# Kernel optimization log

Measured on AMD Instinct MI355X. Metric: run time of the kernel, lower is better.

The kernel has to match this reference:

```python
import jax, jax.numpy as jnp
import numpy as np


def setup_inputs() -> dict:
    key = jax.random.key(0)
    k1, k2, k3 = jax.random.split(key, 3)
    B, S, Q, K, D = 64, 512, 800, 4, 64
    q_data = jax.random.normal(k1, (B, S, Q), dtype=jnp.float32)
    r_data = jax.random.randint(k2, (B, S), 0, K)
    # learned params (xavier-ish scale)
    Wq = jax.random.normal(k3, (D, Q), dtype=jnp.float32) * (0.5 * (2.0 / (Q + D)) ** 0.5)
    bq = jnp.zeros((D,), dtype=jnp.float32)
    Wr = jax.random.normal(jax.random.fold_in(key, 7), (1, K), dtype=jnp.float32) * (0.5 * (2.0 / (K + 1)) ** 0.5)
    br = jnp.zeros((1,), dtype=jnp.float32)
    return {"q_data": q_data, "r_data": r_data, "Wq": Wq, "bq": bq,
            "Wr": Wr, "br": br, "n_questions": Q, "n_cats": K}


def reference(q_data, r_data, Wq, bq, Wr, br, n_questions, n_cats):
    # Vectorized over (batch, seq): original looped over t in python.
    K = n_cats
    k_idx = jnp.arange(K, dtype=q_data.dtype)                      # [K]
    dist = jnp.abs(k_idx[None, None, :] - r_data[..., None].astype(q_data.dtype)) / (K - 1)  # [B,S,K]
    weights = jnp.maximum(1.0 - dist, 0.0)                        # [B,S,K]
    # response_weights: Linear(K -> 1) then sigmoid -> scalar gate per (b,s)
    gate = jax.nn.sigmoid(jnp.einsum('bsk,ok->bso', weights, Wr) + br)  # [B,S,1]
    weighted_q = q_data * gate                                    # [B,S,Q]
    # question_embed: Linear(Q -> D)
    out = jnp.einsum('bsq,dq->bsd', weighted_q, Wq) + bq          # [B,S,D]
    return out
```

## Files before the change

### kernel.cpp

```cpp
#include <hip/hip_runtime.h>
#include <hip/hip_bf16.h>


#define QD 800
#define DD 64
#define M_TOTAL 32768
#define KT 25
#define DEPTH 5

typedef __attribute__((ext_vector_type(8))) short bf16x8;
typedef __attribute__((ext_vector_type(4))) float f32x4;

static __device__ __forceinline__ short f2bf(float f) {
  union { __hip_bfloat16 h; short s; } u;
  u.h = __float2bfloat16(f);
  return u.s;
}

static __device__ __forceinline__ bf16x8 pack8(f32x4 lo, f32x4 hi) {
  bf16x8 r;
  r[0] = f2bf(lo.x); r[1] = f2bf(lo.y); r[2] = f2bf(lo.z); r[3] = f2bf(lo.w);
  r[4] = f2bf(hi.x); r[5] = f2bf(hi.y); r[6] = f2bf(hi.z); r[7] = f2bf(hi.w);
  return r;
}

static __device__ __forceinline__ bf16x8 load_split8(const float* __restrict__ p) {
  return pack8(*reinterpret_cast<const f32x4*>(p),
               *reinterpret_cast<const f32x4*>(p + 16));
}

__global__ void convert_wq_kernel(const float* __restrict__ Wq, short* __restrict__ Bb) {
  int idx = blockIdx.x * 256 + threadIdx.x;
  int kt = idx >> 8;
  int acc = (idx >> 6) & 3;
  int lane = idx & 63;
  int l15 = lane & 15, lhi = lane >> 4;
  const float* p = Wq + (acc * 16 + l15) * QD + kt * 32 + lhi * 4;
  *reinterpret_cast<bf16x8*>(Bb + (size_t)idx * 8) = load_split8(p);
}

__global__ __launch_bounds__(256, 2) void sold_kernel(
    const float* __restrict__ q, const int* __restrict__ rdat,
    const short* __restrict__ Bb, const float* __restrict__ bq,
    const float* __restrict__ Wr, const float* __restrict__ br,
    float* __restrict__ out) {
  const int lane = threadIdx.x & 63;
  const int wave = threadIdx.x >> 6;
  const int l15 = lane & 15;
  const int lhi = lane >> 4;
  const int m0 = blockIdx.x * 64 + wave * 16;

  const float* ap = q + (size_t)(m0 + l15) * QD + lhi * 4;
  const short* bp = Bb + (size_t)lane * 8;

  f32x4 aLo[DEPTH], aHi[DEPTH];
  bf16x8 bfr[DEPTH][4];

#pragma unroll
  for (int s = 0; s < DEPTH; ++s) {
    const float* a = ap + s * 32;
    aLo[s] = *reinterpret_cast<const f32x4*>(a);
    aHi[s] = *reinterpret_cast<const f32x4*>(a + 16);
    const short* p = bp + s * 2048;
    bfr[s][0] = *reinterpret_cast<const bf16x8*>(p + 0 * 512);
    bfr[s][1] = *reinterpret_cast<const bf16x8*>(p + 1 * 512);
    bfr[s][2] = *reinterpret_cast<const bf16x8*>(p + 2 * 512);
    bfr[s][3] = *reinterpret_cast<const bf16x8*>(p + 3 * 512);
  }

  f32x4 acc0 = {0.f, 0.f, 0.f, 0.f};
  f32x4 acc1 = {0.f, 0.f, 0.f, 0.f};
  f32x4 acc2 = {0.f, 0.f, 0.f, 0.f};
  f32x4 acc3 = {0.f, 0.f, 0.f, 0.f};

#pragma unroll
  for (int kt = 0; kt < KT; ++kt) {
    const int s = kt % DEPTH;
    bf16x8 a = pack8(aLo[s], aHi[s]);
    acc0 = __builtin_amdgcn_mfma_f32_16x16x32_bf16(a, bfr[s][0], acc0, 0, 0, 0);
    acc1 = __builtin_amdgcn_mfma_f32_16x16x32_bf16(a, bfr[s][1], acc1, 0, 0, 0);
    acc2 = __builtin_amdgcn_mfma_f32_16x16x32_bf16(a, bfr[s][2], acc2, 0, 0, 0);
    acc3 = __builtin_amdgcn_mfma_f32_16x16x32_bf16(a, bfr[s][3], acc3, 0, 0, 0);
    const int nx = kt + DEPTH;
    if (nx < KT) {
      const float* a2 = ap + nx * 32;
      aLo[s] = *reinterpret_cast<const f32x4*>(a2);
      aHi[s] = *reinterpret_cast<const f32x4*>(a2 + 16);
      const short* p = bp + nx * 2048;
      bfr[s][0] = *reinterpret_cast<const bf16x8*>(p + 0 * 512);
      bfr[s][1] = *reinterpret_cast<const bf16x8*>(p + 1 * 512);
      bfr[s][2] = *reinterpret_cast<const bf16x8*>(p + 2 * 512);
      bfr[s][3] = *reinterpret_cast<const bf16x8*>(p + 3 * 512);
    }
    __builtin_amdgcn_sched_barrier(0);
  }

  float wr[4] = {Wr[0], Wr[1], Wr[2], Wr[3]};
  float brv = br[0];
  float lut[4];
  const float inv3 = 1.0f / 3.0f;
#pragma unroll
  for (int r = 0; r < 4; ++r) {
    float s = brv;
#pragma unroll
    for (int k = 0; k < 4; ++k) {
      float w = fmaxf(1.0f - fabsf((float)(k - r)) * inv3, 0.0f);
      s += w * wr[k];
    }
    lut[r] = 1.0f / (1.0f + __expf(-s));
  }

  float bqv0 = bq[0 * 16 + l15];
  float bqv1 = bq[1 * 16 + l15];
  float bqv2 = bq[2 * 16 + l15];
  float bqv3 = bq[3 * 16 + l15];

#pragma unroll
  for (int r = 0; r < 4; ++r) {
    int row = m0 + lhi * 4 + r;
    float g = lut[rdat[row]];
    float* orow = out + (size_t)row * DD + l15;
    orow[0]  = acc0[r] * g + bqv0;
    orow[16] = acc1[r] * g + bqv1;
    orow[32] = acc2[r] * g + bqv2;
    orow[48] = acc3[r] * g + bqv3;
  }
}

__global__ __launch_bounds__(256, 2) void sold_direct(
    const float* __restrict__ q, const int* __restrict__ rdat,
    const float* __restrict__ Wq, const float* __restrict__ bq,
    const float* __restrict__ Wr, const float* __restrict__ br,
    float* __restrict__ out) {
  const int lane = threadIdx.x & 63;
  const int wave = threadIdx.x >> 6;
  const int l15 = lane & 15;
  const int lhi = lane >> 4;
  const int m0 = blockIdx.x * 64 + wave * 16;
  const float* aptr = q + (size_t)(m0 + l15) * QD + lhi * 4;
  const float* w0 = Wq + (0 * 16 + l15) * QD + lhi * 4;
  const float* w1 = Wq + (1 * 16 + l15) * QD + lhi * 4;
  const float* w2 = Wq + (2 * 16 + l15) * QD + lhi * 4;
  const float* w3 = Wq + (3 * 16 + l15) * QD + lhi * 4;
  f32x4 acc0 = {0.f,0.f,0.f,0.f}, acc1 = {0.f,0.f,0.f,0.f};
  f32x4 acc2 = {0.f,0.f,0.f,0.f}, acc3 = {0.f,0.f,0.f,0.f};
#pragma unroll 5
  for (int kt = 0; kt < KT; ++kt) {
    bf16x8 a  = load_split8(aptr + kt * 32);
    bf16x8 b0 = load_split8(w0 + kt * 32);
    bf16x8 b1 = load_split8(w1 + kt * 32);
    bf16x8 b2 = load_split8(w2 + kt * 32);
    bf16x8 b3 = load_split8(w3 + kt * 32);
    acc0 = __builtin_amdgcn_mfma_f32_16x16x32_bf16(a, b0, acc0, 0, 0, 0);
    acc1 = __builtin_amdgcn_mfma_f32_16x16x32_bf16(a, b1, acc1, 0, 0, 0);
    acc2 = __builtin_amdgcn_mfma_f32_16x16x32_bf16(a, b2, acc2, 0, 0, 0);
    acc3 = __builtin_amdgcn_mfma_f32_16x16x32_bf16(a, b3, acc3, 0, 0, 0);
  }
  float wr[4] = {Wr[0], Wr[1], Wr[2], Wr[3]};
  float brv = br[0], lut[4];
  const float inv3 = 1.0f / 3.0f;
#pragma unroll
  for (int r = 0; r < 4; ++r) {
    float s = brv;
#pragma unroll
    for (int k = 0; k < 4; ++k)
      s += fmaxf(1.0f - fabsf((float)(k - r)) * inv3, 0.0f) * wr[k];
    lut[r] = 1.0f / (1.0f + __expf(-s));
  }
  float bqv0 = bq[l15], bqv1 = bq[16 + l15], bqv2 = bq[32 + l15], bqv3 = bq[48 + l15];
#pragma unroll
  for (int r = 0; r < 4; ++r) {
    int row = m0 + lhi * 4 + r;
    float g = lut[rdat[row]];
    float* orow = out + (size_t)row * DD + l15;
    orow[0]  = acc0[r] * g + bqv0;
    orow[16] = acc1[r] * g + bqv1;
    orow[32] = acc2[r] * g + bqv2;
    orow[48] = acc3[r] * g + bqv3;
  }
}

extern "C" void kernel_launch(void* const* d_in, const int* in_sizes, int n_in,
                              void* d_out, int out_size, void* d_ws, size_t ws_size,
                              hipStream_t stream) {
  const float* q    = (const float*)d_in[0];
  const int*   rdat = (const int*)d_in[1];
  const float* Wq   = (const float*)d_in[2];
  const float* bq   = (const float*)d_in[3];
  const float* Wr   = (const float*)d_in[4];
  const float* br   = (const float*)d_in[5];
  float* out = (float*)d_out;

  const size_t need_ws = (size_t)KT * 2048 * sizeof(short);
  if (ws_size >= need_ws) {
    short* Bb = (short*)d_ws;
    convert_wq_kernel<<<KT, 256, 0, stream>>>(Wq, Bb);
    sold_kernel<<<M_TOTAL / 64, 256, 0, stream>>>(q, rdat, Bb, bq, Wr, br, out);
  } else {
    sold_direct<<<M_TOTAL / 64, 256, 0, stream>>>(q, rdat, Wq, bq, Wr, br, out);
  }
}
```

Before: 169.8 us.

## Split K across two waves per block with 4x4 MFMA tiles and LDS reduction

Each block now uses two waves instead of four. Each wave computes all 64 rows by 64 columns of the block's output tile over half of the K dimension, using 16 accumulators so every loaded B fragment is reused across four row tiles. The two partial sums are combined through shared memory before the gated epilogue. The aim is to cut redundant B-fragment loads, but the change raises register pressure, lowers the wave count per CU, and adds a sync plus a reduction through shared memory.

```diff
diff --git a/kernel.cpp b/kernel.cpp
--- a/kernel.cpp
+++ b/kernel.cpp
@@ -6,7 +6,8 @@
 #define DD 64
 #define M_TOTAL 32768
 #define KT 25
-#define DEPTH 5
+#define KSPLIT 13
+#define DEPTH 3
 
 typedef __attribute__((ext_vector_type(8))) short bf16x8;
 typedef __attribute__((ext_vector_type(4))) float f32x4;
@@ -32,68 +33,111 @@
 __global__ void convert_wq_kernel(const float* __restrict__ Wq, short* __restrict__ Bb) {
   int idx = blockIdx.x * 256 + threadIdx.x;
   int kt = idx >> 8;
-  int acc = (idx >> 6) & 3;
+  int c = (idx >> 6) & 3;
   int lane = idx & 63;
   int l15 = lane & 15, lhi = lane >> 4;
-  const float* p = Wq + (acc * 16 + l15) * QD + kt * 32 + lhi * 4;
+  const float* p = Wq + (c * 16 + l15) * QD + kt * 32 + lhi * 4;
   *reinterpret_cast<bf16x8*>(Bb + (size_t)idx * 8) = load_split8(p);
 }
 
-__global__ __launch_bounds__(256, 2) void sold_kernel(
+template <int CNT>
+static __device__ __forceinline__ void pipe_loop(
+    const float* __restrict__ a0, const float* __restrict__ a1,
+    const float* __restrict__ a2, const float* __restrict__ a3,
+    const short* __restrict__ bp, f32x4 (&acc)[4][4]) {
+  const float* at[4] = {a0, a1, a2, a3};
+  f32x4 sAlo[DEPTH][4], sAhi[DEPTH][4];
+  bf16x8 sB[DEPTH][4];
+
+#pragma unroll
+  for (int s = 0; s < DEPTH; ++s) {
+    if (s < CNT) {
+#pragma unroll
+      for (int t = 0; t < 4; ++t) {
+        sAlo[s][t] = *reinterpret_cast<const f32x4*>(at[t] + s * 32);
+        sAhi[s][t] = *reinterpret_cast<const f32x4*>(at[t] + s * 32 + 16);
+      }
+#pragma unroll
+      for (int c = 0; c < 4; ++c)
+        sB[s][c] = *reinterpret_cast<const bf16x8*>(bp + s * 2048 + c * 512);
+    }
+  }
+
+#pragma unroll
+  for (int kt = 0; kt < CNT; ++kt) {
+    const int s = kt % DEPTH;
+    bf16x8 afr[4];
+#pragma unroll
+    for (int t = 0; t < 4; ++t) afr[t] = pack8(sAlo[s][t], sAhi[s][t]);
+#pragma unroll
+    for (int t = 0; t < 4; ++t)
+#pragma unroll
+      for (int c = 0; c < 4; ++c)
+        acc[t][c] = __builtin_amdgcn_mfma_f32_16x16x32_bf16(afr[t], sB[s][c],
+                                                            acc[t][c], 0, 0, 0);
+    const int nx = kt + DEPTH;
+    if (nx < CNT) {
+#pragma unroll
+      for (int t = 0; t < 4; ++t) {
+        sAlo[s][t] = *reinterpret_cast<const f32x4*>(at[t] + nx * 32);
+        sAhi[s][t] = *reinterpret_cast<const f32x4*>(at[t] + nx * 32 + 16);
+      }
+#pragma unroll
+      for (int c = 0; c < 4; ++c)
+        sB[s][c] = *reinterpret_cast<const bf16x8*>(bp + nx * 2048 + c * 512);
+    }
+    __builtin_amdgcn_sched_barrier(0);
+  }
+}
+
+__global__ __launch_bounds__(128, 1) void sold_kernel(
     const float* __restrict__ q, const int* __restrict__ rdat,
     const short* __restrict__ Bb, const float* __restrict__ bq,
     const float* __restrict__ Wr, const float* __restrict__ br,
     float* __restrict__ out) {
   const int lane = threadIdx.x & 63;
-  const int wave = threadIdx.x >> 6;
+  const int khalf = threadIdx.x >> 6;
   const int l15 = lane & 15;
   const int lhi = lane >> 4;
-  const int m0 = blockIdx.x * 64 + wave * 16;
-
-  const float* ap = q + (size_t)(m0 + l15) * QD + lhi * 4;
-  const short* bp = Bb + (size_t)lane * 8;
-
-  f32x4 aLo[DEPTH], aHi[DEPTH];
-  bf16x8 bfr[DEPTH][4];
-
-#pragma unroll
-  for (int s = 0; s < DEPTH; ++s) {
-    const float* a = ap + s * 32;
-    aLo[s] = *reinterpret_cast<const f32x4*>(a);
-    aHi[s] = *reinterpret_cast<const f32x4*>(a + 16);
-    const short* p = bp + s * 2048;
-    bfr[s][0] = *reinterpret_cast<const bf16x8*>(p + 0 * 512);
-    bfr[s][1] = *reinterpret_cast<const bf16x8*>(p + 1 * 512);
-    bfr[s][2] = *reinterpret_cast<const bf16x8*>(p + 2 * 512);
-    bfr[s][3] = *reinterpret_cast<const bf16x8*>(p + 3 * 512);
-  }
-
-  f32x4 acc0 = {0.f, 0.f, 0.f, 0.f};
-  f32x4 acc1 = {0.f, 0.f, 0.f, 0.f};
-  f32x4 acc2 = {0.f, 0.f, 0.f, 0.f};
-  f32x4 acc3 = {0.f, 0.f, 0.f, 0.f};
-
-#pragma unroll
-  for (int kt = 0; kt < KT; ++kt) {
-    const int s = kt % DEPTH;
-    bf16x8 a = pack8(aLo[s], aHi[s]);
-    acc0 = __builtin_amdgcn_mfma_f32_16x16x32_bf16(a, bfr[s][0], acc0, 0, 0, 0);
-    acc1 = __builtin_amdgcn_mfma_f32_16x16x32_bf16(a, bfr[s][1], acc1, 0, 0, 0);
-    acc2 = __builtin_amdgcn_mfma_f32_16x16x32_bf16(a, bfr[s][2], acc2, 0, 0, 0);
-    acc3 = __builtin_amdgcn_mfma_f32_16x16x32_bf16(a, bfr[s][3], acc3, 0, 0, 0);
-    const int nx = kt + DEPTH;
-    if (nx < KT) {
-      const float* a2 = ap + nx * 32;
-      aLo[s] = *reinterpret_cast<const f32x4*>(a2);
-      aHi[s] = *reinterpret_cast<const f32x4*>(a2 + 16);
-      const short* p = bp + nx * 2048;
-      bfr[s][0] = *reinterpret_cast<const bf16x8*>(p + 0 * 512);
-      bfr[s][1] = *reinterpret_cast<const bf16x8*>(p + 1 * 512);
-      bfr[s][2] = *reinterpret_cast<const bf16x8*>(p + 2 * 512);
-      bfr[s][3] = *reinterpret_cast<const bf16x8*>(p + 3 * 512);
-    }
-    __builtin_amdgcn_sched_barrier(0);
-  }
+  const int m0 = blockIdx.x * 64;
+  const int kt0 = khalf ? KSPLIT : 0;
+
+  const float* a0 = q + (size_t)(m0 +  0 + l15) * QD + kt0 * 32 + lhi * 4;
+  const float* a1 = q + (size_t)(m0 + 16 + l15) * QD + kt0 * 32 + lhi * 4;
+  const float* a2 = q + (size_t)(m0 + 32 + l15) * QD + kt0 * 32 + lhi * 4;
+  const float* a3 = q + (size_t)(m0 + 48 + l15) * QD + kt0 * 32 + lhi * 4;
+  const short* bp = Bb + (size_t)kt0 * 2048 + lane * 8;
+
+  f32x4 acc[4][4];
+#pragma unroll
+  for (int t = 0; t < 4; ++t)
+#pragma unroll
+    for (int c = 0; c < 4; ++c) acc[t][c] = {0.f, 0.f, 0.f, 0.f};
+
+  if (khalf == 0) {
+    pipe_loop<KSPLIT>(a0, a1, a2, a3, bp, acc);
+  } else {
+    pipe_loop<KT - KSPLIT>(a0, a1, a2, a3, bp, acc);
+  }
+
+  __shared__ float comb[4][16][64];
+  if (khalf == 1) {
+#pragma unroll
+    for (int t = 0; t < 4; ++t)
+#pragma unroll
+      for (int c = 0; c < 4; ++c)
+#pragma unroll
+        for (int r = 0; r < 4; ++r) comb[t][c * 4 + r][lane] = acc[t][c][r];
+  }
+  __syncthreads();
+  if (khalf == 1) return;
+
+#pragma unroll
+  for (int t = 0; t < 4; ++t)
+#pragma unroll
+    for (int c = 0; c < 4; ++c)
+#pragma unroll
+      for (int r = 0; r < 4; ++r) acc[t][c][r] += comb[t][c * 4 + r][lane];
 
   float wr[4] = {Wr[0], Wr[1], Wr[2], Wr[3]};
   float brv = br[0];
@@ -103,27 +147,25 @@
   for (int r = 0; r < 4; ++r) {
     float s = brv;
 #pragma unroll
-    for (int k = 0; k < 4; ++k) {
-      float w = fmaxf(1.0f - fabsf((float)(k - r)) * inv3, 0.0f);
-      s += w * wr[k];
+    for (int k = 0; k < 4; ++k)
+      s += fmaxf(1.0f - fabsf((float)(k - r)) * inv3, 0.0f) * wr[k];
+    lut[r] = 1.0f / (1.0f + __expf(-s));
+  }
+
+  float bqv[4];
+#pragma unroll
+  for (int c = 0; c < 4; ++c) bqv[c] = bq[c * 16 + l15];
+
+#pragma unroll
+  for (int t = 0; t < 4; ++t) {
+#pragma unroll
+    for (int r = 0; r < 4; ++r) {
+      int row = m0 + t * 16 + lhi * 4 + r;
+      float g = lut[rdat[row]];
+      float* orow = out + (size_t)row * DD + l15;
+#pragma unroll
+      for (int c = 0; c < 4; ++c) orow[c * 16] = acc[t][c][r] * g + bqv[c];
     }
-    lut[r] = 1.0f / (1.0f + __expf(-s));
-  }
-
-  float bqv0 = bq[0 * 16 + l15];
-  float bqv1 = bq[1 * 16 + l15];
-  float bqv2 = bq[2 * 16 + l15];
-  float bqv3 = bq[3 * 16 + l15];
-
-#pragma unroll
-  for (int r = 0; r < 4; ++r) {
-    int row = m0 + lhi * 4 + r;
-    float g = lut[rdat[row]];
-    float* orow = out + (size_t)row * DD + l15;
-    orow[0]  = acc0[r] * g + bqv0;
-    orow[16] = acc1[r] * g + bqv1;
-    orow[32] = acc2[r] * g + bqv2;
-    orow[48] = acc3[r] * g + bqv3;
   }
 }
 
@@ -195,7 +237,7 @@
   if (ws_size >= need_ws) {
     short* Bb = (short*)d_ws;
     convert_wq_kernel<<<KT, 256, 0, stream>>>(Wq, Bb);
-    sold_kernel<<<M_TOTAL / 64, 256, 0, stream>>>(q, rdat, Bb, bq, Wr, br, out);
+    sold_kernel<<<M_TOTAL / 64, 128, 0, stream>>>(q, rdat, Bb, bq, Wr, br, out);
   } else {
     sold_direct<<<M_TOTAL / 64, 256, 0, stream>>>(q, rdat, Wq, bq, Wr, br, out);
   }
```

Measured after the change: 171.2 us. About the same (+0.9%).
